# Performance work log

Hardware: AMD Instinct MI355X
Metric: run time of the kernel (lower is better)

Reference implementation:

```python
import jax, jax.numpy as jnp
import numpy as np

B, S, D, HD, NH = 1, 2048, 1024, 64, 16
INV_SQRT = 1.0 / HD ** 0.5


def _rope_tables(seq_len, head_dim):
    inv_freq = 1.0 / 10000.0 ** (np.arange(0, head_dim, 2, dtype=np.float32) / head_dim)
    t = np.arange(seq_len, dtype=np.float32)
    freqs = t[:, None] * inv_freq[None, :]            # [S, HD/2]
    emb = np.concatenate([freqs, freqs], axis=1)      # [S, HD]
    cos = jnp.asarray(np.cos(emb), dtype=jnp.float32)[None, :, :, None]  # [1,S,HD,1]
    sin = jnp.asarray(np.sin(emb), dtype=jnp.float32)[None, :, :, None]
    return cos, sin

COS, SIN = _rope_tables(S, HD)


def _rotate_half(x):
    # NB: faithful to original torch code: chunk on LAST axis, which is the HEADS axis here
    x1, x2 = jnp.split(x, 2, axis=-1)
    return jnp.concatenate([-x2, x1], axis=-1)


def setup_inputs() -> dict:
    key = jax.random.key(0)
    ks = jax.random.split(key, 8)
    x = jax.random.normal(ks[0], (B, S, D), dtype=jnp.float32)
    bias = jax.random.normal(ks[1], (B, S, S, NH), dtype=jnp.float32)
    mask = jax.random.randint(ks[2], (B, S, S, NH), 0, 2, dtype=jnp.int32)
    w_qkv = jax.random.normal(ks[3], (3 * NH * HD, D), dtype=jnp.float32) * 0.02
    b_qkv = jnp.zeros((3 * NH * HD,), dtype=jnp.float32)
    w_out = jax.random.normal(ks[4], (D, NH * HD), dtype=jnp.float32) * 0.02
    b_out = jnp.zeros((D,), dtype=jnp.float32)
    return {"x": x, "bias": bias, "mask": mask, "w_qkv": w_qkv, "b_qkv": b_qkv,
            "w_out": w_out, "b_out": b_out}


def reference(x, bias, mask, w_qkv, b_qkv, w_out, b_out):
    qkv = x @ w_qkv.T + b_qkv                         # [B,S,3*NH*HD]
    q, k, v = jnp.split(qkv, 3, axis=-1)
    # torch .view((..., head_dim, n_heads)): last dim splits row-major into (HD, NH)
    q = q.reshape(B, S, HD, NH)
    k = k.reshape(B, S, HD, NH)
    v = v.reshape(B, S, HD, NH)
    # inline RoPE (rotate_half over the heads axis, as in the original code)
    cos = COS[:, :S]
    sin = SIN[:, :S]
    q = q * cos + _rotate_half(q) * sin
    k = k * cos + _rotate_half(k) * sin
    attn_score = INV_SQRT * jnp.einsum('bjdh,bkdh->bjkh', q, k)  # [B,S,S,NH]
    attn_score = attn_score + bias
    attn_score = jnp.where(mask == 0, jnp.float32(-1e8), attn_score)
    attn_logits = jax.nn.softmax(attn_score, axis=2)
    attn = jnp.einsum('bjkh,bkdh->bjdh', attn_logits, v)          # [B,S,HD,NH]
    out = attn.reshape(B, S, HD * NH) @ w_out.T + b_out           # [B,S,D]
    return out
```

## Files before the change

kernel.cpp:

```cpp
#include <hip/hip_runtime.h>
#include <stdint.h>
#include <math.h>

using f32x4  = __attribute__((ext_vector_type(4)))  float;
using f32x16 = __attribute__((ext_vector_type(16))) float;
using s16x8  = __attribute__((ext_vector_type(8)))  short;

#define DI __device__ __forceinline__

DI unsigned short f2bf(float f) {
  unsigned u = __float_as_uint(f);
  u += 0x7FFFu + ((u >> 16) & 1u);
  return (unsigned short)(u >> 16);
}
DI float bf2f(unsigned short h) { return __uint_as_float((unsigned)h << 16); }

__global__ void k_cvt_bf16(const float* __restrict__ in, unsigned short* __restrict__ out, int n4) {
  int i = blockIdx.x * blockDim.x + threadIdx.x;
  const int stride = gridDim.x * blockDim.x;
  for (; i < n4; i += stride) {
    float4 v = reinterpret_cast<const float4*>(in)[i];
    ushort4 o;
    o.x = f2bf(v.x); o.y = f2bf(v.y); o.z = f2bf(v.z); o.w = f2bf(v.w);
    reinterpret_cast<ushort4*>(out)[i] = o;
  }
}

__global__ void k_rope_table(float* __restrict__ cost, float* __restrict__ sint) {
  const int idx = blockIdx.x * 256 + threadIdx.x;
  const int s = idx >> 5, fi = idx & 31;
  const double invf = pow(10000.0, -(double)fi / 32.0);
  const float ang = (float)s * (float)invf;
  cost[idx] = (float)cos((double)ang);
  sint[idx] = (float)sin((double)ang);
}

__global__ __launch_bounds__(256) void k_gemm_bt(
    const unsigned short* __restrict__ A, const unsigned short* __restrict__ B,
    const float* __restrict__ bias, float* __restrict__ C, int M, int N, int K) {
  __shared__ unsigned short As[128 * 32], Bs[128 * 32];
  const int tid = threadIdx.x, l = tid & 63, w = tid >> 6;
  const int wr = w >> 1, wc = w & 1;
  const int m0 = blockIdx.x * 128, n0 = blockIdx.y * 128;
  const int srow = tid >> 2, scol = (tid & 3) * 8;
  f32x4 acc[4][4] = {};
  for (int k0 = 0; k0 < K; k0 += 32) {
    s16x8 a0 = *(const s16x8*)(A + (size_t)(m0 + srow) * K + k0 + scol);
    s16x8 a1 = *(const s16x8*)(A + (size_t)(m0 + 64 + srow) * K + k0 + scol);
    s16x8 b0 = *(const s16x8*)(B + (size_t)(n0 + srow) * K + k0 + scol);
    s16x8 b1 = *(const s16x8*)(B + (size_t)(n0 + 64 + srow) * K + k0 + scol);
    __syncthreads();
    *(s16x8*)&As[srow * 32 + scol] = a0;
    *(s16x8*)&As[(64 + srow) * 32 + scol] = a1;
    *(s16x8*)&Bs[srow * 32 + scol] = b0;
    *(s16x8*)&Bs[(64 + srow) * 32 + scol] = b1;
    __syncthreads();
    s16x8 af[4], bf[4];
#pragma unroll
    for (int i = 0; i < 4; i++)
      af[i] = *(const s16x8*)&As[(wr * 64 + i * 16 + (l & 15)) * 32 + (l >> 4) * 8];
#pragma unroll
    for (int j = 0; j < 4; j++)
      bf[j] = *(const s16x8*)&Bs[(wc * 64 + j * 16 + (l & 15)) * 32 + (l >> 4) * 8];
#pragma unroll
    for (int i = 0; i < 4; i++)
#pragma unroll
      for (int j = 0; j < 4; j++)
        acc[i][j] = __builtin_amdgcn_mfma_f32_16x16x32_bf16(af[i], bf[j], acc[i][j], 0, 0, 0);
  }
#pragma unroll
  for (int i = 0; i < 4; i++) {
    const int row = m0 + wr * 64 + i * 16 + (l >> 4) * 4;
#pragma unroll
    for (int j = 0; j < 4; j++) {
      const int col = n0 + wc * 64 + j * 16 + (l & 15);
      const float bv = bias ? bias[col] : 0.f;
#pragma unroll
      for (int r = 0; r < 4; r++) C[(size_t)(row + r) * N + col] = acc[i][j][r] + bv;
    }
  }
}

__global__ void k_rope_relayout(const float* __restrict__ qkv, const float* __restrict__ cost,
                                const float* __restrict__ sint,
                                unsigned short* __restrict__ qh, unsigned short* __restrict__ kh,
                                unsigned short* __restrict__ vt) {
  const int s = blockIdx.x, t = threadIdx.x;
  const float* row = qkv + (size_t)s * 3072;
  const int c = t * 4;
  const int d = c >> 4;
  const int hbase = c & 15;
  const float cv = cost[s * 32 + (d & 31)];
  const float sv = sint[s * 32 + (d & 31)];
  const float sgn = (hbase < 8) ? -1.f : 1.f;
  {
    float4 v = *(const float4*)(row + c);
    float4 v2 = *(const float4*)(row + (c ^ 8));
    const float* vp = (const float*)&v;
    const float* vp2 = (const float*)&v2;
#pragma unroll
    for (int i = 0; i < 4; i++) {
      float val = vp[i] * cv + sgn * vp2[i] * sv;
      qh[(size_t)(hbase + i) * (2048 * 64) + s * 64 + d] = f2bf(val);
    }
  }
  {
    float4 v = *(const float4*)(row + 1024 + c);
    float4 v2 = *(const float4*)(row + 1024 + (c ^ 8));
    const float* vp = (const float*)&v;
    const float* vp2 = (const float*)&v2;
#pragma unroll
    for (int i = 0; i < 4; i++) {
      float val = vp[i] * cv + sgn * vp2[i] * sv;
      kh[(size_t)(hbase + i) * (2048 * 64) + s * 64 + d] = f2bf(val);
    }
  }
  {
    float4 v = *(const float4*)(row + 2048 + c);
    const float* vp = (const float*)&v;
#pragma unroll
    for (int i = 0; i < 4; i++)
      vt[(size_t)(hbase + i) * (64 * 2048) + (size_t)d * 2048 + s] = f2bf(vp[i]);
  }
}

struct Stage {
  float4 b0, b1, b2, b3;
  int4 m0, m1, m2, m3;
};

DI void stage_load(Stage& st, const float* bp0, const float* bp1,
                   const int* mp0, const int* mp1, int it) {
  const size_t off = (size_t)it * 512;
  st.b0 = *(const float4*)(bp0 + off);
  st.b1 = *(const float4*)(bp0 + off + 4);
  st.b2 = *(const float4*)(bp1 + off);
  st.b3 = *(const float4*)(bp1 + off + 4);
  st.m0 = *(const int4*)(mp0 + off);
  st.m1 = *(const int4*)(mp0 + off + 4);
  st.m2 = *(const int4*)(mp1 + off);
  st.m3 = *(const int4*)(mp1 + off + 4);
}

DI void stage_write4(unsigned short* dst, const float4& b, const int4& m, int hrbase) {
  const float* bv = (const float*)&b;
  const int* mv = (const int*)&m;
#pragma unroll
  for (int q = 0; q < 4; q++)
    dst[(hrbase + q) * 34] = f2bf(mv[q] ? bv[q] : -1.0e8f);
}

DI void stage_write(const Stage& st, unsigned short* bm, int kr, int jr) {
  unsigned short* d0 = bm + (kr * 8) * 34 + jr;
  stage_write4(d0, st.b0, st.m0, 0);
  stage_write4(d0, st.b1, st.m1, 4);
  unsigned short* d1 = d0 + 16;
  stage_write4(d1, st.b2, st.m2, 0);
  stage_write4(d1, st.b3, st.m3, 4);
}

DI void load_kv(s16x8 (&kf)[4], s16x8 (&vf)[4],
                const unsigned short* kb, const unsigned short* vb, int it) {
  const unsigned short* kp = kb + (size_t)it * (32 * 64);
#pragma unroll
  for (int ds = 0; ds < 4; ds++) kf[ds] = *(const s16x8*)(kp + ds * 16);
  const unsigned short* vp = vb + (size_t)it * 32;
  vf[0] = *(const s16x8*)(vp);
  vf[1] = *(const s16x8*)(vp + 32 * 2048);
  vf[2] = *(const s16x8*)(vp + 16);
  vf[3] = *(const s16x8*)(vp + 32 * 2048 + 16);
}

DI void attn_step(const s16x8 (&kf)[4], const s16x8 (&vf)[4], const s16x8 (&qf)[4],
                  const unsigned short* bm, int hi, int ln, int w,
                  f32x16& o0, f32x16& o1, float& mrun, float& lrun) {
  f32x16 st = {};
#pragma unroll
  for (int ds = 0; ds < 4; ds++)
    st = __builtin_amdgcn_mfma_f32_32x32x16_bf16(kf[ds], qf[ds], st, 0, 0, 0);
  float p[16];
  float tmax = -3.0e38f;
#pragma unroll
  for (int r = 0; r < 16; r++) {
    const int kl = (r & 3) + 8 * (r >> 2) + 4 * hi;
    const float b = bf2f(bm[(kl * 8 + w) * 34 + ln]);
    const float sv = st[r] * 0.125f + b;
    p[r] = sv;
    tmax = fmaxf(tmax, sv);
  }
  tmax = fmaxf(tmax, __shfl_xor(tmax, 32));
  const float mnew = fmaxf(mrun, tmax);
  const float sc = __expf(mrun - mnew);
  float psum = 0.f;
#pragma unroll
  for (int r = 0; r < 16; r++) { p[r] = __expf(p[r] - mnew); psum += p[r]; }
  psum += __shfl_xor(psum, 32);
  lrun = lrun * sc + psum;
  mrun = mnew;
#pragma unroll
  for (int r = 0; r < 16; r++) {
    const int jj = (r & 3) + 8 * (r >> 2) + 4 * hi;
    const float s2 = __shfl(sc, jj);
    o0[r] *= s2;
    o1[r] *= s2;
  }
  unsigned pk[8];
#pragma unroll
  for (int q = 0; q < 8; q++)
    pk[q] = (unsigned)f2bf(p[2 * q]) | ((unsigned)f2bf(p[2 * q + 1]) << 16);
#pragma unroll
  for (int s = 0; s < 2; s++) {
    const unsigned a0 = pk[4 * s + 0], a1 = pk[4 * s + 1];
    const unsigned a2 = pk[4 * s + 2], a3 = pk[4 * s + 3];
    const unsigned x0 = (unsigned)__shfl_xor((int)a0, 32);
    const unsigned x1 = (unsigned)__shfl_xor((int)a1, 32);
    const unsigned x2 = (unsigned)__shfl_xor((int)a2, 32);
    const unsigned x3 = (unsigned)__shfl_xor((int)a3, 32);
    union { int4 i; s16x8 v; } u;
    u.i.x = (int)(hi ? x2 : a0);
    u.i.y = (int)(hi ? x3 : a1);
    u.i.z = (int)(hi ? a2 : x0);
    u.i.w = (int)(hi ? a3 : x1);
    o0 = __builtin_amdgcn_mfma_f32_32x32x16_bf16(u.v, vf[2 * s + 0], o0, 0, 0, 0);
    o1 = __builtin_amdgcn_mfma_f32_32x32x16_bf16(u.v, vf[2 * s + 1], o1, 0, 0, 0);
  }
}

__global__ __launch_bounds__(512) void k_attn(
    const float* __restrict__ bias, const int* __restrict__ mask,
    const unsigned short* __restrict__ qh, const unsigned short* __restrict__ kh,
    const unsigned short* __restrict__ vt,
    float* __restrict__ Opart, float* __restrict__ ML) {
  const int tid = threadIdx.x, l = tid & 63, w = tid >> 6;
  const int hi = l >> 5, ln = l & 31;
  const int hg = blockIdx.x, jt = blockIdx.y, ks = blockIdx.z;
  const int j0 = jt * 32, h = hg * 8 + w, kstart = ks * 512;
  __shared__ unsigned short bm[32 * 8 * 34];

  s16x8 qf[4];
  {
    const unsigned short* qb = qh + ((size_t)h * 2048 + (j0 + ln)) * 64 + 8 * hi;
#pragma unroll
    for (int ds = 0; ds < 4; ds++) qf[ds] = *(const s16x8*)(qb + ds * 16);
  }

  const int kr = (l & 3) + 4 * w;
  const int jr = (l >> 2) & 15;
  const size_t rowstep = (size_t)2048 * 16;
  const size_t base0 = ((size_t)(j0 + jr) * 2048 + (kstart + kr)) * 16 + hg * 8;
  const float* bp0 = bias + base0;
  const float* bp1 = bp0 + 16 * rowstep;
  const int* mp0 = mask + base0;
  const int* mp1 = mp0 + 16 * rowstep;

  const unsigned short* kb = kh + ((size_t)h * 2048 + (kstart + ln)) * 64 + 8 * hi;
  const unsigned short* vb = vt + (size_t)h * 64 * 2048 + (size_t)ln * 2048 + kstart + 8 * hi;

  f32x16 o0 = {}, o1 = {};
  float mrun = -3.0e38f, lrun = 0.f;

  Stage sA, sB;
  s16x8 kfA[4], vfA[4], kfB[4], vfB[4];
  stage_load(sA, bp0, bp1, mp0, mp1, 0);
  load_kv(kfA, vfA, kb, vb, 0);

  for (int it = 0; it < 16; it += 2) {
    stage_write(sA, bm, kr, jr);
    __syncthreads();
    stage_load(sB, bp0, bp1, mp0, mp1, it + 1);
    load_kv(kfB, vfB, kb, vb, it + 1);
    attn_step(kfA, vfA, qf, bm, hi, ln, w, o0, o1, mrun, lrun);
    __syncthreads();
    stage_write(sB, bm, kr, jr);
    __syncthreads();
    if (it + 2 < 16) {
      stage_load(sA, bp0, bp1, mp0, mp1, it + 2);
      load_kv(kfA, vfA, kb, vb, it + 2);
    }
    attn_step(kfB, vfB, qf, bm, hi, ln, w, o0, o1, mrun, lrun);
    __syncthreads();
  }

  float* ob = Opart + ((((size_t)ks * 64 + jt) * 2 + hg) * 32) * 512;
#pragma unroll
  for (int r = 0; r < 16; r++) {
    const int jj = (r & 3) + 8 * (r >> 2) + 4 * hi;
    ob[(size_t)jj * 512 + w * 64 + ln] = o0[r];
    ob[(size_t)jj * 512 + w * 64 + 32 + ln] = o1[r];
  }
  if (hi == 0) {
    float* mlp = ML + (((((size_t)ks * 64 + jt) * 2 + hg) * 32 + ln) * 8 + w) * 2;
    mlp[0] = mrun;
    mlp[1] = lrun;
  }
}

__global__ void k_combine(const float* __restrict__ Opart, const float* __restrict__ ML,
                          unsigned short* __restrict__ attn_flat) {
  const int j = blockIdx.x, t = threadIdx.x;
  const int jt = j >> 5, jl = j & 31;
  const int d = t >> 2;
  const size_t base2 = ((size_t)jt * 2) * 32 + jl;
  unsigned short tmp[4];
#pragma unroll
  for (int q = 0; q < 4; q++) {
    const int hh = 4 * (t & 3) + q;
    const int hg = hh >> 3, hl = hh & 7;
    const size_t slotb = base2 + (size_t)hg * 32;
    float m[4], lv[4];
#pragma unroll
    for (int ksi = 0; ksi < 4; ksi++) {
      const float* mlp = ML + (((size_t)ksi * 4096 + slotb) * 8 + hl) * 2;
      m[ksi] = mlp[0];
      lv[ksi] = mlp[1];
    }
    const float M = fmaxf(fmaxf(m[0], m[1]), fmaxf(m[2], m[3]));
    float L = 0.f, acc = 0.f;
#pragma unroll
    for (int ksi = 0; ksi < 4; ksi++) {
      const float e = __expf(m[ksi] - M);
      L += lv[ksi] * e;
      acc += Opart[((size_t)ksi * 4096 + slotb) * 512 + hl * 64 + d] * e;
    }
    tmp[q] = f2bf(acc / L);
  }
  ushort4 outv;
  outv.x = tmp[0]; outv.y = tmp[1]; outv.z = tmp[2]; outv.w = tmp[3];
  *(ushort4*)(attn_flat + (size_t)j * 1024 + t * 4) = outv;
}

extern "C" void kernel_launch(void* const* d_in, const int* in_sizes, int n_in,
                              void* d_out, int out_size, void* d_ws, size_t ws_size,
                              hipStream_t stream) {
  const float* x     = (const float*)d_in[0];
  const float* bias  = (const float*)d_in[1];
  const int*   mask  = (const int*)d_in[2];
  const float* w_qkv = (const float*)d_in[3];
  const float* b_qkv = (const float*)d_in[4];
  const float* w_out = (const float*)d_in[5];
  const float* b_out = (const float*)d_in[6];
  float* out = (float*)d_out;

  char* ws = (char*)d_ws;
  unsigned short* xb   = (unsigned short*)(ws);
  unsigned short* wqb  = (unsigned short*)(ws + ((size_t)4 << 20));
  unsigned short* wob  = (unsigned short*)(ws + ((size_t)10 << 20));
  float* cost          = (float*)(ws + ((size_t)12 << 20));
  float* sint          = (float*)(ws + ((size_t)12 << 20) + (256 << 10));
  float* qkv           = (float*)(ws + ((size_t)13 << 20));
  unsigned short* qhp  = (unsigned short*)(ws + ((size_t)37 << 20));
  unsigned short* khp  = (unsigned short*)(ws + ((size_t)41 << 20));
  unsigned short* vtp  = (unsigned short*)(ws + ((size_t)45 << 20));
  unsigned short* af   = (unsigned short*)(ws + ((size_t)49 << 20));
  float* Opart         = (float*)(ws + ((size_t)53 << 20));
  float* ML            = (float*)(ws + ((size_t)85 << 20));

  k_cvt_bf16<<<dim3(512), dim3(256), 0, stream>>>(x, xb, 2048 * 1024 / 4);
  k_cvt_bf16<<<dim3(512), dim3(256), 0, stream>>>(w_qkv, wqb, 3072 * 1024 / 4);
  k_cvt_bf16<<<dim3(512), dim3(256), 0, stream>>>(w_out, wob, 1024 * 1024 / 4);
  k_rope_table<<<dim3(256), dim3(256), 0, stream>>>(cost, sint);
  k_gemm_bt<<<dim3(16, 24), dim3(256), 0, stream>>>(xb, wqb, b_qkv, qkv, 2048, 3072, 1024);
  k_rope_relayout<<<dim3(2048), dim3(256), 0, stream>>>(qkv, cost, sint, qhp, khp, vtp);
  k_attn<<<dim3(2, 64, 4), dim3(512), 0, stream>>>(bias, mask, qhp, khp, vtp, Opart, ML);
  k_combine<<<dim3(2048), dim3(256), 0, stream>>>(Opart, ML, af);
  k_gemm_bt<<<dim3(16, 8), dim3(256), 0, stream>>>(af, wob, b_out, out, 2048, 1024, 1024);
}
```

Before: 324.3 us.

## Pre-pack masked bias into bf16 MFMA-fragment layout in separate prep kernel

Adds a k_prep kernel that merges bias and mask into a bf16 tensor laid out per head so each attention lane can fetch its score-fragment values with uint2 loads. The attention kernel drops its shared-memory bias staging and barriers, shrinks to 256-thread blocks with 4 heads each, and prefetches the next step's bias from global memory. Opart and ML are re-laid out per head to match, and k_combine is updated accordingly. This removes the LDS round trip and syncs from the hot loop, at the cost of an extra kernel launch that writes and rereads a 128 MB bf16 intermediate.

Result: slower. 415.2 us (+28.1%).

```diff
diff --git a/kernel.cpp b/kernel.cpp
--- a/kernel.cpp
+++ b/kernel.cpp
@@ -124,118 +124,52 @@
   }
 }
 
-struct Stage {
-  float4 b0, b1, b2, b3;
-  int4 m0, m1, m2, m3;
-};
-
-DI void stage_load(Stage& st, const float* bp0, const float* bp1,
-                   const int* mp0, const int* mp1, int it) {
-  const size_t off = (size_t)it * 512;
-  st.b0 = *(const float4*)(bp0 + off);
-  st.b1 = *(const float4*)(bp0 + off + 4);
-  st.b2 = *(const float4*)(bp1 + off);
-  st.b3 = *(const float4*)(bp1 + off + 4);
-  st.m0 = *(const int4*)(mp0 + off);
-  st.m1 = *(const int4*)(mp0 + off + 4);
-  st.m2 = *(const int4*)(mp1 + off);
-  st.m3 = *(const int4*)(mp1 + off + 4);
-}
-
-DI void stage_write4(unsigned short* dst, const float4& b, const int4& m, int hrbase) {
-  const float* bv = (const float*)&b;
-  const int* mv = (const int*)&m;
-#pragma unroll
-  for (int q = 0; q < 4; q++)
-    dst[(hrbase + q) * 34] = f2bf(mv[q] ? bv[q] : -1.0e8f);
-}
-
-DI void stage_write(const Stage& st, unsigned short* bm, int kr, int jr) {
-  unsigned short* d0 = bm + (kr * 8) * 34 + jr;
-  stage_write4(d0, st.b0, st.m0, 0);
-  stage_write4(d0, st.b1, st.m1, 4);
-  unsigned short* d1 = d0 + 16;
-  stage_write4(d1, st.b2, st.m2, 0);
-  stage_write4(d1, st.b3, st.m3, 4);
-}
-
-DI void load_kv(s16x8 (&kf)[4], s16x8 (&vf)[4],
-                const unsigned short* kb, const unsigned short* vb, int it) {
-  const unsigned short* kp = kb + (size_t)it * (32 * 64);
-#pragma unroll
-  for (int ds = 0; ds < 4; ds++) kf[ds] = *(const s16x8*)(kp + ds * 16);
-  const unsigned short* vp = vb + (size_t)it * 32;
-  vf[0] = *(const s16x8*)(vp);
-  vf[1] = *(const s16x8*)(vp + 32 * 2048);
-  vf[2] = *(const s16x8*)(vp + 16);
-  vf[3] = *(const s16x8*)(vp + 32 * 2048 + 16);
-}
-
-DI void attn_step(const s16x8 (&kf)[4], const s16x8 (&vf)[4], const s16x8 (&qf)[4],
-                  const unsigned short* bm, int hi, int ln, int w,
-                  f32x16& o0, f32x16& o1, float& mrun, float& lrun) {
-  f32x16 st = {};
-#pragma unroll
-  for (int ds = 0; ds < 4; ds++)
-    st = __builtin_amdgcn_mfma_f32_32x32x16_bf16(kf[ds], qf[ds], st, 0, 0, 0);
-  float p[16];
-  float tmax = -3.0e38f;
-#pragma unroll
-  for (int r = 0; r < 16; r++) {
-    const int kl = (r & 3) + 8 * (r >> 2) + 4 * hi;
-    const float b = bf2f(bm[(kl * 8 + w) * 34 + ln]);
-    const float sv = st[r] * 0.125f + b;
-    p[r] = sv;
-    tmax = fmaxf(tmax, sv);
-  }
-  tmax = fmaxf(tmax, __shfl_xor(tmax, 32));
-  const float mnew = fmaxf(mrun, tmax);
-  const float sc = __expf(mrun - mnew);
-  float psum = 0.f;
-#pragma unroll
-  for (int r = 0; r < 16; r++) { p[r] = __expf(p[r] - mnew); psum += p[r]; }
-  psum += __shfl_xor(psum, 32);
-  lrun = lrun * sc + psum;
-  mrun = mnew;
-#pragma unroll
-  for (int r = 0; r < 16; r++) {
-    const int jj = (r & 3) + 8 * (r >> 2) + 4 * hi;
-    const float s2 = __shfl(sc, jj);
-    o0[r] *= s2;
-    o1[r] *= s2;
-  }
-  unsigned pk[8];
-#pragma unroll
-  for (int q = 0; q < 8; q++)
-    pk[q] = (unsigned)f2bf(p[2 * q]) | ((unsigned)f2bf(p[2 * q + 1]) << 16);
-#pragma unroll
-  for (int s = 0; s < 2; s++) {
-    const unsigned a0 = pk[4 * s + 0], a1 = pk[4 * s + 1];
-    const unsigned a2 = pk[4 * s + 2], a3 = pk[4 * s + 3];
-    const unsigned x0 = (unsigned)__shfl_xor((int)a0, 32);
-    const unsigned x1 = (unsigned)__shfl_xor((int)a1, 32);
-    const unsigned x2 = (unsigned)__shfl_xor((int)a2, 32);
-    const unsigned x3 = (unsigned)__shfl_xor((int)a3, 32);
-    union { int4 i; s16x8 v; } u;
-    u.i.x = (int)(hi ? x2 : a0);
-    u.i.y = (int)(hi ? x3 : a1);
-    u.i.z = (int)(hi ? a2 : x0);
-    u.i.w = (int)(hi ? a3 : x1);
-    o0 = __builtin_amdgcn_mfma_f32_32x32x16_bf16(u.v, vf[2 * s + 0], o0, 0, 0, 0);
-    o1 = __builtin_amdgcn_mfma_f32_32x32x16_bf16(u.v, vf[2 * s + 1], o1, 0, 0, 0);
-  }
-}
-
-__global__ __launch_bounds__(512) void k_attn(
-    const float* __restrict__ bias, const int* __restrict__ mask,
+#define PH 1092
+__global__ __launch_bounds__(256) void k_prep(const float* __restrict__ bias,
+                                              const int* __restrict__ mask,
+                                              unsigned short* __restrict__ bmG) {
+  __shared__ unsigned short lds[16 * PH];
+  const int t = threadIdx.x;
+  const int j0 = blockIdx.x * 32, k0 = blockIdx.y * 32;
+  const int j_r = t >> 3;
+  const size_t rowbase = ((size_t)(j0 + j_r) * 2048 + k0) * 16;
+  const float* bro = bias + rowbase;
+  const int* mro = mask + rowbase;
+#pragma unroll
+  for (int i = 0; i < 16; ++i) {
+    const int f = (t & 7) + 8 * i;
+    float4 bv = *(const float4*)(bro + f * 4);
+    int4 mv = *(const int4*)(mro + f * 4);
+    const int k_l = f >> 2, h0 = 4 * (f & 3);
+    const float* bvp = (const float*)&bv;
+    const int* mvp = (const int*)&mv;
+#pragma unroll
+    for (int e = 0; e < 4; ++e)
+      lds[(h0 + e) * PH + j_r * 34 + k_l] = f2bf(mvp[e] ? bvp[e] : -1.0e8f);
+  }
+  __syncthreads();
+  const int rc = t >> 1, half = t & 1;
+  const int hh = rc >> 3, ko_l = rc & 7;
+  unsigned short* outp = bmG + (((size_t)hh * 512 + (size_t)(k0 >> 2) + ko_l) * 2048 + j0 + half * 16) * 4;
+  const unsigned short* lp = &lds[hh * PH + (half * 16) * 34 + 4 * ko_l];
+#pragma unroll
+  for (int s = 0; s < 8; ++s) {
+    uint2 a = *(const uint2*)(lp + (2 * s) * 34);
+    uint2 b = *(const uint2*)(lp + (2 * s + 1) * 34);
+    uint4 o; o.x = a.x; o.y = a.y; o.z = b.x; o.w = b.y;
+    *(uint4*)(outp + (2 * s) * 4) = o;
+  }
+}
+
+__global__ __launch_bounds__(256, 3) void k_attn(
+    const unsigned short* __restrict__ bmG,
     const unsigned short* __restrict__ qh, const unsigned short* __restrict__ kh,
     const unsigned short* __restrict__ vt,
     float* __restrict__ Opart, float* __restrict__ ML) {
   const int tid = threadIdx.x, l = tid & 63, w = tid >> 6;
   const int hi = l >> 5, ln = l & 31;
-  const int hg = blockIdx.x, jt = blockIdx.y, ks = blockIdx.z;
-  const int j0 = jt * 32, h = hg * 8 + w, kstart = ks * 512;
-  __shared__ unsigned short bm[32 * 8 * 34];
+  const int q4 = blockIdx.x, jt = blockIdx.y, ks = blockIdx.z;
+  const int j0 = jt * 32, h = q4 * 4 + w, kstart = ks * 512;
 
   s16x8 qf[4];
   {
@@ -243,53 +177,97 @@
 #pragma unroll
     for (int ds = 0; ds < 4; ds++) qf[ds] = *(const s16x8*)(qb + ds * 16);
   }
-
-  const int kr = (l & 3) + 4 * w;
-  const int jr = (l >> 2) & 15;
-  const size_t rowstep = (size_t)2048 * 16;
-  const size_t base0 = ((size_t)(j0 + jr) * 2048 + (kstart + kr)) * 16 + hg * 8;
-  const float* bp0 = bias + base0;
-  const float* bp1 = bp0 + 16 * rowstep;
-  const int* mp0 = mask + base0;
-  const int* mp1 = mp0 + 16 * rowstep;
-
   const unsigned short* kb = kh + ((size_t)h * 2048 + (kstart + ln)) * 64 + 8 * hi;
   const unsigned short* vb = vt + (size_t)h * 64 * 2048 + (size_t)ln * 2048 + kstart + 8 * hi;
+  const uint2* bp = (const uint2*)bmG + ((size_t)h * 512 + (size_t)ks * 128 + hi) * 2048 + j0 + ln;
 
   f32x16 o0 = {}, o1 = {};
   float mrun = -3.0e38f, lrun = 0.f;
 
-  Stage sA, sB;
-  s16x8 kfA[4], vfA[4], kfB[4], vfB[4];
-  stage_load(sA, bp0, bp1, mp0, mp1, 0);
-  load_kv(kfA, vfA, kb, vb, 0);
-
-  for (int it = 0; it < 16; it += 2) {
-    stage_write(sA, bm, kr, jr);
-    __syncthreads();
-    stage_load(sB, bp0, bp1, mp0, mp1, it + 1);
-    load_kv(kfB, vfB, kb, vb, it + 1);
-    attn_step(kfA, vfA, qf, bm, hi, ln, w, o0, o1, mrun, lrun);
-    __syncthreads();
-    stage_write(sB, bm, kr, jr);
-    __syncthreads();
-    if (it + 2 < 16) {
-      stage_load(sA, bp0, bp1, mp0, mp1, it + 2);
-      load_kv(kfA, vfA, kb, vb, it + 2);
-    }
-    attn_step(kfB, vfB, qf, bm, hi, ln, w, o0, o1, mrun, lrun);
-    __syncthreads();
-  }
-
-  float* ob = Opart + ((((size_t)ks * 64 + jt) * 2 + hg) * 32) * 512;
+  uint2 bnx[4];
+#pragma unroll
+  for (int c = 0; c < 4; c++) bnx[c] = bp[(size_t)(2 * c) * 2048];
+
+  for (int it = 0; it < 16; ++it) {
+    uint2 bcur[4];
+#pragma unroll
+    for (int c = 0; c < 4; c++) bcur[c] = bnx[c];
+    if (it + 1 < 16) {
+#pragma unroll
+      for (int c = 0; c < 4; c++) bnx[c] = bp[(size_t)((it + 1) * 8 + 2 * c) * 2048];
+    }
+    s16x8 kf[4], vf[4];
+    {
+      const unsigned short* kp = kb + (size_t)it * (32 * 64);
+#pragma unroll
+      for (int ds = 0; ds < 4; ds++) kf[ds] = *(const s16x8*)(kp + ds * 16);
+      const unsigned short* vp = vb + (size_t)it * 32;
+      vf[0] = *(const s16x8*)(vp);
+      vf[1] = *(const s16x8*)(vp + 32 * 2048);
+      vf[2] = *(const s16x8*)(vp + 16);
+      vf[3] = *(const s16x8*)(vp + 32 * 2048 + 16);
+    }
+    f32x16 st = {};
+#pragma unroll
+    for (int ds = 0; ds < 4; ds++)
+      st = __builtin_amdgcn_mfma_f32_32x32x16_bf16(kf[ds], qf[ds], st, 0, 0, 0);
+    float p[16];
+    float tmax = -3.0e38f;
+#pragma unroll
+    for (int r = 0; r < 16; r++) {
+      const unsigned word = (r & 2) ? bcur[r >> 2].y : bcur[r >> 2].x;
+      const unsigned short u = (r & 1) ? (unsigned short)(word >> 16) : (unsigned short)(word & 0xffffu);
+      const float sv = st[r] * 0.125f + bf2f(u);
+      p[r] = sv;
+      tmax = fmaxf(tmax, sv);
+    }
+    tmax = fmaxf(tmax, __shfl_xor(tmax, 32));
+    const float mnew = fmaxf(mrun, tmax);
+    const float sc = __expf(mrun - mnew);
+    float psum = 0.f;
+#pragma unroll
+    for (int r = 0; r < 16; r++) { p[r] = __expf(p[r] - mnew); psum += p[r]; }
+    psum += __shfl_xor(psum, 32);
+    lrun = lrun * sc + psum;
+    mrun = mnew;
+#pragma unroll
+    for (int r = 0; r < 16; r++) {
+      const int jj = (r & 3) + 8 * (r >> 2) + 4 * hi;
+      const float s2 = __shfl(sc, jj);
+      o0[r] *= s2;
+      o1[r] *= s2;
+    }
+    unsigned pk[8];
+#pragma unroll
+    for (int q = 0; q < 8; q++)
+      pk[q] = (unsigned)f2bf(p[2 * q]) | ((unsigned)f2bf(p[2 * q + 1]) << 16);
+#pragma unroll
+    for (int s = 0; s < 2; s++) {
+      const unsigned a0 = pk[4 * s + 0], a1 = pk[4 * s + 1];
+      const unsigned a2 = pk[4 * s + 2], a3 = pk[4 * s + 3];
+      const unsigned x0 = (unsigned)__shfl_xor((int)a0, 32);
+      const unsigned x1 = (unsigned)__shfl_xor((int)a1, 32);
+      const unsigned x2 = (unsigned)__shfl_xor((int)a2, 32);
+      const unsigned x3 = (unsigned)__shfl_xor((int)a3, 32);
+      union { int4 i; s16x8 v; } u;
+      u.i.x = (int)(hi ? x2 : a0);
+      u.i.y = (int)(hi ? x3 : a1);
+      u.i.z = (int)(hi ? a2 : x0);
+      u.i.w = (int)(hi ? a3 : x1);
+      o0 = __builtin_amdgcn_mfma_f32_32x32x16_bf16(u.v, vf[2 * s + 0], o0, 0, 0, 0);
+      o1 = __builtin_amdgcn_mfma_f32_32x32x16_bf16(u.v, vf[2 * s + 1], o1, 0, 0, 0);
+    }
+  }
+
+  float* ob = Opart + (((size_t)(ks * 64 + jt) * 16 + h) * 32) * 64;
 #pragma unroll
   for (int r = 0; r < 16; r++) {
     const int jj = (r & 3) + 8 * (r >> 2) + 4 * hi;
-    ob[(size_t)jj * 512 + w * 64 + ln] = o0[r];
-    ob[(size_t)jj * 512 + w * 64 + 32 + ln] = o1[r];
+    ob[(size_t)jj * 64 + ln] = o0[r];
+    ob[(size_t)jj * 64 + 32 + ln] = o1[r];
   }
   if (hi == 0) {
-    float* mlp = ML + (((((size_t)ks * 64 + jt) * 2 + hg) * 32 + ln) * 8 + w) * 2;
+    float* mlp = ML + (((size_t)(ks * 64 + jt) * 16 + h) * 32 + ln) * 2;
     mlp[0] = mrun;
     mlp[1] = lrun;
   }
@@ -300,19 +278,16 @@
   const int j = blockIdx.x, t = threadIdx.x;
   const int jt = j >> 5, jl = j & 31;
   const int d = t >> 2;
-  const size_t base2 = ((size_t)jt * 2) * 32 + jl;
   unsigned short tmp[4];
 #pragma unroll
   for (int q = 0; q < 4; q++) {
     const int hh = 4 * (t & 3) + q;
-    const int hg = hh >> 3, hl = hh & 7;
-    const size_t slotb = base2 + (size_t)hg * 32;
     float m[4], lv[4];
 #pragma unroll
     for (int ksi = 0; ksi < 4; ksi++) {
-      const float* mlp = ML + (((size_t)ksi * 4096 + slotb) * 8 + hl) * 2;
-      m[ksi] = mlp[0];
-      lv[ksi] = mlp[1];
+      const size_t base = ((size_t)(ksi * 64 + jt) * 16 + hh) * 32 + jl;
+      m[ksi] = ML[base * 2];
+      lv[ksi] = ML[base * 2 + 1];
     }
     const float M = fmaxf(fmaxf(m[0], m[1]), fmaxf(m[2], m[3]));
     float L = 0.f, acc = 0.f;
@@ -320,7 +295,8 @@
     for (int ksi = 0; ksi < 4; ksi++) {
       const float e = __expf(m[ksi] - M);
       L += lv[ksi] * e;
-      acc += Opart[((size_t)ksi * 4096 + slotb) * 512 + hl * 64 + d] * e;
+      const size_t base = ((size_t)(ksi * 64 + jt) * 16 + hh) * 32 + jl;
+      acc += Opart[base * 64 + d] * e;
     }
     tmp[q] = f2bf(acc / L);
   }
@@ -353,15 +329,17 @@
   unsigned short* vtp  = (unsigned short*)(ws + ((size_t)45 << 20));
   unsigned short* af   = (unsigned short*)(ws + ((size_t)49 << 20));
   float* Opart         = (float*)(ws + ((size_t)53 << 20));
-  float* ML            = (float*)(ws + ((size_t)85 << 20));
+  float* ML            = (float*)(ws + ((size_t)88 << 20));
+  unsigned short* bmG  = (unsigned short*)(ws + ((size_t)90 << 20));
 
   k_cvt_bf16<<<dim3(512), dim3(256), 0, stream>>>(x, xb, 2048 * 1024 / 4);
   k_cvt_bf16<<<dim3(512), dim3(256), 0, stream>>>(w_qkv, wqb, 3072 * 1024 / 4);
   k_cvt_bf16<<<dim3(512), dim3(256), 0, stream>>>(w_out, wob, 1024 * 1024 / 4);
   k_rope_table<<<dim3(256), dim3(256), 0, stream>>>(cost, sint);
+  k_prep<<<dim3(64, 64), dim3(256), 0, stream>>>(bias, mask, bmG);
   k_gemm_bt<<<dim3(16, 24), dim3(256), 0, stream>>>(xb, wqb, b_qkv, qkv, 2048, 3072, 1024);
   k_rope_relayout<<<dim3(2048), dim3(256), 0, stream>>>(qkv, cost, sint, qhp, khp, vtp);
-  k_attn<<<dim3(2, 64, 4), dim3(512), 0, stream>>>(bias, mask, qhp, khp, vtp, Opart, ML);
+  k_attn<<<dim3(4, 64, 4), dim3(256), 0, stream>>>(bmG, qhp, khp, vtp, Opart, ML);
   k_combine<<<dim3(2048), dim3(256), 0, stream>>>(Opart, ML, af);
   k_gemm_bt<<<dim3(16, 8), dim3(256), 0, stream>>>(af, wob, b_out, out, 2048, 1024, 1024);
 }
```
